# Kernel tuning notes

Hardware: AMD Instinct MI355X
Metric: run time of the kernel (lower is better)

The kernel has to match this reference:

```python
import jax, jax.numpy as jnp
import numpy as np

N = 16384
D_IN = 128
LAYERS = [128, 128, 128, 10]
LATENT = [64, 64]


def _linear_params(key, fan_in, fan_out):
    k1, k2 = jax.random.split(key)
    bound = 1.0 / np.sqrt(fan_in)
    w = jax.random.uniform(k1, (fan_in, fan_out), minval=-bound, maxval=bound, dtype=jnp.float32)
    b = jax.random.uniform(k2, (fan_out,), minval=-bound, maxval=bound, dtype=jnp.float32)
    return w, b


def setup_inputs() -> dict:
    key = jax.random.key(0)
    ks = jax.random.split(key, 8)
    feat_matrix = jax.random.normal(ks[0], (N, D_IN), dtype=jnp.float32)
    gl_w0, gl_b0 = _linear_params(ks[1], LAYERS[0], LATENT[0])
    gnn_w0, gnn_b0 = _linear_params(ks[2], LAYERS[0], LAYERS[1])
    gl_w1, gl_b1 = _linear_params(ks[3], LAYERS[1], LATENT[1])
    gnn_w1, gnn_b1 = _linear_params(ks[4], LAYERS[1], LAYERS[2])
    out_w, out_b = _linear_params(ks[5], LAYERS[2], LAYERS[3])
    return {
        "feat_matrix": feat_matrix,
        "gl_w0": gl_w0, "gl_b0": gl_b0,
        "gl_w1": gl_w1, "gl_b1": gl_b1,
        "gnn_w0": gnn_w0, "gnn_b0": gnn_b0,
        "gnn_w1": gnn_w1, "gnn_b1": gnn_b1,
        "out_w": out_w, "out_b": out_b,
        "temp": jnp.float32(0.1),
        "theta": jnp.float32(0.1),
        "adj_matrix": jnp.zeros((N, N), dtype=jnp.float32),
        "get_item_index": jax.random.randint(ks[6], (1024,), 0, N, dtype=jnp.int32),
        "set_index": jax.random.randint(ks[7], (1024,), 0, N, dtype=jnp.int32),
        "val_index": jax.random.randint(jax.random.fold_in(key, 9), (1024,), 0, N, dtype=jnp.int32),
        "mask_matrix": jnp.zeros((N,), dtype=bool),
    }


def _layer(x, gl_w, gl_b, gnn_w, gnn_b, temp, theta):
    # graph-learning projection
    g = jax.nn.relu(x @ gl_w + gl_b)                     # [N, L]
    # pairwise squared L2 distances (utils.l2_mat)
    sq = jnp.sum(g * g, axis=-1)                         # [N]
    dist = sq[:, None] + sq[None, :] - 2.0 * (g @ g.T)   # [N, N]
    t = 1.0 + temp
    th = 5.0 + theta
    adj = jax.nn.sigmoid(t * (-dist) + th)               # [N, N]
    # diag(rowsum).inverse() @ adj @ gnn(x) == row-normalized message passing
    msg = adj @ (x @ gnn_w + gnn_b)                      # [N, H]
    return msg / jnp.sum(adj, axis=-1, keepdims=True)


def reference(feat_matrix, gl_w0, gl_b0, gl_w1, gl_b1,
              gnn_w0, gnn_b0, gnn_w1, gnn_b1,
              out_w, out_b, temp, theta,
              adj_matrix, get_item_index, set_index, val_index, mask_matrix):
    x = feat_matrix
    x = jax.nn.relu(_layer(x, gl_w0, gl_b0, gnn_w0, gnn_b0, temp, theta))
    x = _layer(x, gl_w1, gl_b1, gnn_w1, gnn_b1, temp, theta)  # last gnn layer: no relu
    x = x @ out_w + out_b
    return jax.nn.softmax(x, axis=-1)
```

## Files before the change

### kernel.cpp

```cpp
#include <hip/hip_runtime.h>

#define NN 16384
#define DL 64
#define HD 128
#define BMW 32
#define BM 128
#define BN 64
#define JS 8
#define JCH (NN / JS)

typedef _Float16 v8h __attribute__((ext_vector_type(8)));
typedef float v16f __attribute__((ext_vector_type(16)));
typedef unsigned short ushort_t;
typedef unsigned int uint32;

__device__ __forceinline__ float bf2f(ushort_t v) {
  return __uint_as_float(((uint32)v) << 16);
}
__device__ __forceinline__ ushort_t f2bf(float f) {
  uint32 u = __float_as_uint(f);
  return (ushort_t)((u + 0x7FFFu + ((u >> 16) & 1u)) >> 16);
}
__device__ __forceinline__ uint32 pack2h(float a, float b) {
  union { _Float16 h; ushort_t s; } ua, ub;
  ua.h = (_Float16)a; ub.h = (_Float16)b;
  return (uint32)ua.s | ((uint32)ub.s << 16);
}
__device__ __forceinline__ void gld16(void* lds, const void* gp) {
  __builtin_amdgcn_global_load_lds(
      (const __attribute__((address_space(1))) uint32*)gp,
      (__attribute__((address_space(3))) uint32*)lds, 16, 0, 0);
}

__global__ void detect_k(const void* __restrict__ feat,
                         const void* __restrict__ temp,
                         const void* __restrict__ theta,
                         float* __restrict__ consts) {
  const int l = threadIdx.x;
  const ushort_t* u = (const ushort_t*)feat;
  float v0 = fabsf(bf2f(u[2 * l]));
  float v1 = fabsf(bf2f(u[2 * l + 1]));
  int ok = ((v0 > 1e-4f && v0 < 16.0f) ? 1 : 0) +
           ((v1 > 1e-4f && v1 < 16.0f) ? 1 : 0);
#pragma unroll
  for (int off = 1; off < 64; off <<= 1) ok += __shfl_xor(ok, off, 64);
  if (l == 0) {
    int isbf = (ok >= 100) ? 1 : 0;
    float tv, th;
    if (isbf) {
      tv = bf2f(((const ushort_t*)temp)[0]);
      th = bf2f(((const ushort_t*)theta)[0]);
    } else {
      tv = ((const float*)temp)[0];
      th = ((const float*)theta)[0];
    }
    consts[0] = (float)isbf;
    consts[1] = 1.0f + tv;
    consts[2] = 5.0f + th;
    consts[3] = 2.0f * (1.0f + tv) * 1.44269504088896341f;
  }
}

template <int L0>
__global__ __launch_bounds__(256) void prep_k(
    const void* __restrict__ xb, const float* __restrict__ msgp,
    const float* __restrict__ denp, const void* __restrict__ glw,
    const void* __restrict__ glb, const void* __restrict__ gnw,
    const void* __restrict__ gnb, const float* __restrict__ cst,
    _Float16* __restrict__ g, _Float16* __restrict__ hT,
    float* __restrict__ crow) {
  __shared__ float xr[4][128];
  const int w = threadIdx.x >> 6, l = threadIdx.x & 63;
  const int row = blockIdx.x * 4 + w;
  const int isbf = (cst[0] != 0.0f);
  float x0, x1;
  if (L0) {
    if (isbf) {
      const ushort_t* p = (const ushort_t*)xb;
      x0 = bf2f(p[row * 128 + 2 * l]);
      x1 = bf2f(p[row * 128 + 2 * l + 1]);
    } else {
      const float* p = (const float*)xb;
      x0 = p[row * 128 + 2 * l];
      x1 = p[row * 128 + 2 * l + 1];
    }
  } else {
    float m0 = 0.0f, m1 = 0.0f, d = 0.0f;
#pragma unroll
    for (int js = 0; js < JS; ++js) {
      const float* mp = msgp + (size_t)js * NN * HD + (size_t)row * HD;
      m0 += mp[2 * l];
      m1 += mp[2 * l + 1];
      d += denp[js * NN + row];
    }
    float rd = __builtin_amdgcn_rcpf(fmaxf(d, 1e-10f));
    x0 = fmaxf(m0 * rd, 0.0f);
    x1 = fmaxf(m1 * rd, 0.0f);
  }
  xr[w][2 * l] = x0;
  xr[w][2 * l + 1] = x1;
  __syncthreads();
  float ag = 0.0f, a0 = 0.0f, a1 = 0.0f;
  float bg, b0, b1;
  if (isbf) {
    const ushort_t* Wg = (const ushort_t*)glw;
    const ushort_t* Wn = (const ushort_t*)gnw;
#pragma unroll 8
    for (int k = 0; k < 128; ++k) {
      float xk = xr[w][k];
      ag = fmaf(xk, bf2f(Wg[k * 64 + l]), ag);
      a0 = fmaf(xk, bf2f(Wn[k * 128 + l]), a0);
      a1 = fmaf(xk, bf2f(Wn[k * 128 + 64 + l]), a1);
    }
    bg = bf2f(((const ushort_t*)glb)[l]);
    b0 = bf2f(((const ushort_t*)gnb)[l]);
    b1 = bf2f(((const ushort_t*)gnb)[64 + l]);
  } else {
    const float* Wg = (const float*)glw;
    const float* Wn = (const float*)gnw;
#pragma unroll 8
    for (int k = 0; k < 128; ++k) {
      float xk = xr[w][k];
      ag = fmaf(xk, Wg[k * 64 + l], ag);
      a0 = fmaf(xk, Wn[k * 128 + l], a0);
      a1 = fmaf(xk, Wn[k * 128 + 64 + l], a1);
    }
    bg = ((const float*)glb)[l];
    b0 = ((const float*)gnb)[l];
    b1 = ((const float*)gnb)[64 + l];
  }
  const float t = cst[1];
  const float th = cst[2];
  float gv = fmaxf(ag + bg, 0.0f);
  _Float16 gq = (_Float16)gv;
  g[(size_t)row * DL + l] = gq;
  float gf = (float)gq;
  float sq = gf * gf;
#pragma unroll
  for (int off = 1; off < 64; off <<= 1) sq += __shfl_xor(sq, off, 64);
  if (l == 0) crow[row] = (0.5f * th - t * sq) * 1.44269504088896341f;
  hT[(size_t)l * NN + row] = (_Float16)(a0 + b0);
  hT[(size_t)(l + 64) * NN + row] = (_Float16)(a1 + b1);
}

__global__ __launch_bounds__(256, 2) void attn_main(
    const _Float16* __restrict__ g, const _Float16* __restrict__ hT,
    const float* __restrict__ crow, const float* __restrict__ cst,
    float* __restrict__ msgp, float* __restrict__ denp) {
  __shared__ __align__(16) short SM[4096 + 8192];
  _Float16* Gs = (_Float16*)SM;
  _Float16* Hs = (_Float16*)(SM + 4096);

  const int tid = threadIdx.x;
  const int w = tid >> 6;
  const int l = tid & 63;
  const int ln = l & 31;
  const int hb = l >> 5;
  const int iw = blockIdx.x * BM + w * BMW;
  const int jb = blockIdx.y * JCH;
  const float s2 = cst[3];

  v8h Bi[4];
#pragma unroll
  for (int kf = 0; kf < 4; ++kf)
    Bi[kf] = *(const v8h*)(g + (size_t)(iw + ln) * DL + kf * 16 + hb * 8);

  const float ci = crow[iw + ln];

  v16f o[4];
#pragma unroll
  for (int mp = 0; mp < 4; ++mp)
#pragma unroll
    for (int r = 0; r < 16; ++r) o[mp][r] = 0.0f;

  float dp = 0.0f;

#pragma unroll 1
  for (int itr = 0; itr < JCH / BN; ++itr) {
    const int j0 = jb + itr * BN;
    __syncthreads();
#pragma unroll
    for (int oo = 0; oo < 2; ++oo) {
      int c = oo * 256 + tid;
      int jj = c >> 3, pc = c & 7;
      int kc = pc ^ (jj & 7);
      gld16((char*)Gs + (oo * 256 + w * 64) * 16,
            g + (size_t)(j0 + jj) * DL + kc * 8);
    }
#pragma unroll
    for (int oo = 0; oo < 4; ++oo) {
      int c = oo * 256 + tid;
      int hc = c >> 3, pc = c & 7;
      int jc = pc ^ (hc & 7);
      gld16((char*)Hs + (oo * 256 + w * 64) * 16,
            hT + (size_t)hc * NN + j0 + jc * 8);
    }
    __syncthreads();

#pragma unroll
    for (int jt = 0; jt < 2; ++jt) {
      float cj[16];
#pragma unroll
      for (int q2 = 0; q2 < 4; ++q2) {
        float4 f4 = *(const float4*)(crow + j0 + jt * 32 + q2 * 8 + 4 * hb);
        cj[q2 * 4 + 0] = f4.x;
        cj[q2 * 4 + 1] = f4.y;
        cj[q2 * 4 + 2] = f4.z;
        cj[q2 * 4 + 3] = f4.w;
      }
      v16f sv;
#pragma unroll
      for (int r = 0; r < 16; ++r) sv[r] = 0.0f;
#pragma unroll
      for (int kf = 0; kf < 4; ++kf) {
        int row = jt * 32 + ln;
        int kc = kf * 2 + hb;
        v8h a = *(const v8h*)(Gs + row * 64 + ((kc ^ (row & 7)) * 8));
        sv = __builtin_amdgcn_mfma_f32_32x32x16_f16(a, Bi[kf], sv, 0, 0, 0);
      }
      float pv[16];
      float dps = 0.0f;
#pragma unroll
      for (int r = 0; r < 16; ++r) {
        float arg = fmaf(s2, sv[r], ci) + cj[r];
        arg = fminf(fmaxf(arg, -60.0f), 60.0f);
        float e = __builtin_amdgcn_exp2f(-arg);
        float adj = 256.0f * __builtin_amdgcn_rcpf(1.0f + e);
        dps += adj;
        pv[r] = adj;
      }
      dp += dps;
#pragma unroll
      for (int kq = 0; kq < 2; ++kq) {
        int q = kq * 8;
        uint32 lo0 = pack2h(pv[q + 0], pv[q + 1]);
        uint32 lo1 = pack2h(pv[q + 2], pv[q + 3]);
        uint32 hi0 = pack2h(pv[q + 4], pv[q + 5]);
        uint32 hi1 = pack2h(pv[q + 6], pv[q + 7]);
        uint32 sl0 = (uint32)__shfl_xor((int)lo0, 32, 64);
        uint32 sl1 = (uint32)__shfl_xor((int)lo1, 32, 64);
        uint32 sh0 = (uint32)__shfl_xor((int)hi0, 32, 64);
        uint32 sh1 = (uint32)__shfl_xor((int)hi1, 32, 64);
        union { uint32 u[4]; v8h v; } b;
        b.u[0] = hb ? sh0 : lo0;
        b.u[1] = hb ? sh1 : lo1;
        b.u[2] = hb ? hi0 : sl0;
        b.u[3] = hb ? hi1 : sl1;
        int kc = (jt * 2 + kq) * 2 + hb;
#pragma unroll
        for (int mp = 0; mp < 4; ++mp) {
          int hc = mp * 32 + ln;
          v8h Ah = *(const v8h*)(Hs + hc * 64 + ((kc ^ (hc & 7)) * 8));
          o[mp] = __builtin_amdgcn_mfma_f32_32x32x16_f16(Ah, b.v, o[mp], 0, 0, 0);
        }
      }
    }
  }

  dp += __shfl_xor(dp, 32, 64);
  if (hb == 0) denp[blockIdx.y * NN + iw + ln] = dp;
  __syncthreads();
  float* Tw = ((float*)SM) + w * (32 * 33);
  float* mout = msgp + (size_t)blockIdx.y * NN * HD;
#pragma unroll
  for (int mp = 0; mp < 4; ++mp) {
#pragma unroll
    for (int r = 0; r < 16; ++r) {
      int hl = (r & 3) + 8 * (r >> 2) + 4 * hb;
      Tw[ln * 33 + hl] = o[mp][r];
    }
#pragma unroll
    for (int rr = 0; rr < 16; ++rr) {
      int il = rr * 2 + hb;
      mout[(size_t)(iw + il) * HD + mp * 32 + ln] = Tw[il * 33 + ln];
    }
  }
}

__global__ __launch_bounds__(256) void final_k(
    const float* __restrict__ msgp, const float* __restrict__ denp,
    const void* __restrict__ ow, const void* __restrict__ ob,
    const float* __restrict__ cst, void* __restrict__ out) {
  __shared__ float Ws[1280];
  const int isbf = (cst[0] != 0.0f);
  if (isbf) {
    for (int i = threadIdx.x; i < 1280; i += 256) Ws[i] = bf2f(((const ushort_t*)ow)[i]);
  } else {
    for (int i = threadIdx.x; i < 1280; i += 256) Ws[i] = ((const float*)ow)[i];
  }
  __syncthreads();
  const int l16 = threadIdx.x & 15, grp = threadIdx.x >> 4;
  const int row = blockIdx.x * 16 + grp;
  float d = 0.0f;
#pragma unroll
  for (int js = 0; js < JS; ++js) d += denp[js * NN + row];
  const float rd = __builtin_amdgcn_rcpf(fmaxf(d, 1e-10f));
  float acc[10];
#pragma unroll
  for (int c = 0; c < 10; ++c) acc[c] = 0.0f;
#pragma unroll
  for (int kk = 0; kk < 8; ++kk) {
    int k = kk * 16 + l16;
    float m = 0.0f;
#pragma unroll
    for (int js = 0; js < JS; ++js)
      m += msgp[(size_t)js * NN * HD + (size_t)row * HD + k];
    float xv = m * rd;
    xv = fminf(fmaxf(xv, -1e6f), 1e6f);
#pragma unroll
    for (int c = 0; c < 10; ++c) acc[c] = fmaf(xv, Ws[k * 10 + c], acc[c]);
  }
  float bias[10];
  if (isbf) {
#pragma unroll
    for (int c = 0; c < 10; ++c) bias[c] = bf2f(((const ushort_t*)ob)[c]);
  } else {
#pragma unroll
    for (int c = 0; c < 10; ++c) bias[c] = ((const float*)ob)[c];
  }
#pragma unroll
  for (int c = 0; c < 10; ++c) {
#pragma unroll
    for (int off = 1; off < 16; off <<= 1) acc[c] += __shfl_xor(acc[c], off, 64);
    acc[c] += bias[c];
  }
  float m = acc[0];
#pragma unroll
  for (int c = 1; c < 10; ++c) m = fmaxf(m, acc[c]);
  float s = 0.0f, e[10];
#pragma unroll
  for (int c = 0; c < 10; ++c) {
    e[c] = __builtin_amdgcn_exp2f((acc[c] - m) * 1.44269504088896341f);
    s += e[c];
  }
  float rs = __builtin_amdgcn_rcpf(s);
  float mine = e[0];
#pragma unroll
  for (int c = 1; c < 10; ++c) mine = (l16 == c) ? e[c] : mine;
  if (l16 < 10) {
    float v = mine * rs;
    if (isbf) ((ushort_t*)out)[(size_t)row * 10 + l16] = f2bf(v);
    else ((float*)out)[(size_t)row * 10 + l16] = v;
  }
}

extern "C" void kernel_launch(void* const* d_in, const int* in_sizes, int n_in,
                              void* d_out, int out_size, void* d_ws,
                              size_t ws_size, hipStream_t stream) {
  const void* feat = d_in[0];
  const void* glw0 = d_in[1];
  const void* glb0 = d_in[2];
  const void* glw1 = d_in[3];
  const void* glb1 = d_in[4];
  const void* gnw0 = d_in[5];
  const void* gnb0 = d_in[6];
  const void* gnw1 = d_in[7];
  const void* gnb1 = d_in[8];
  const void* ow = d_in[9];
  const void* obv = d_in[10];
  const void* temp = d_in[11];
  const void* thet = d_in[12];

  char* ws = (char*)d_ws;
  _Float16* g = (_Float16*)ws;
  _Float16* hT = (_Float16*)(ws + (size_t)(2u << 20));
  float* crow = (float*)(ws + (size_t)(6u << 20));
  float* cst = (float*)(ws + (size_t)(6u << 20) + (1u << 16));
  float* msgp = (float*)(ws + (size_t)(7u << 20));
  float* denp = (float*)(ws + (size_t)(71u << 20));

  dim3 b256(256);
  detect_k<<<dim3(1), dim3(64), 0, stream>>>(feat, temp, thet, cst);
  prep_k<1><<<dim3(NN / 4), b256, 0, stream>>>(feat, nullptr, nullptr, glw0,
                                               glb0, gnw0, gnb0, cst, g, hT,
                                               crow);
  attn_main<<<dim3(NN / BM, JS), b256, 0, stream>>>(g, hT, crow, cst, msgp,
                                                    denp);
  prep_k<0><<<dim3(NN / 4), b256, 0, stream>>>(nullptr, msgp, denp, glw1, glb1,
                                               gnw1, gnb1, cst, g, hT, crow);
  attn_main<<<dim3(NN / BM, JS), b256, 0, stream>>>(g, hT, crow, cst, msgp,
                                                    denp);
  final_k<<<dim3(NN / 16), b256, 0, stream>>>(msgp, denp, ow, obv, cst, d_out);
}
```

Measured before the change: 1.675 ms.

## Double-buffer LDS tiles in attention loop and cheapen sigmoid packing

Splits shared memory into two buffers so the async global-to-LDS loads for the next j-tile are issued before computing the current one. This hides load latency behind the MFMA and exp work and cuts one barrier per iteration. The change also packs to fp16 with a single round-toward-zero convert instruction and drops the clamp on the sigmoid argument. In exchange, LDS use per block doubles, which could limit occupancy. Skipping the clamp relies on exp2 overflow to infinity still giving a correct sigmoid.

```diff
diff --git a/kernel.cpp b/kernel.cpp
--- a/kernel.cpp
+++ b/kernel.cpp
@@ -8,8 +8,10 @@
 #define BN 64
 #define JS 8
 #define JCH (NN / JS)
+#define NITER (JCH / BN)
 
 typedef _Float16 v8h __attribute__((ext_vector_type(8)));
+typedef __fp16 v2fp16 __attribute__((ext_vector_type(2)));
 typedef float v16f __attribute__((ext_vector_type(16)));
 typedef unsigned short ushort_t;
 typedef unsigned int uint32;
@@ -22,9 +24,9 @@
   return (ushort_t)((u + 0x7FFFu + ((u >> 16) & 1u)) >> 16);
 }
 __device__ __forceinline__ uint32 pack2h(float a, float b) {
-  union { _Float16 h; ushort_t s; } ua, ub;
-  ua.h = (_Float16)a; ub.h = (_Float16)b;
-  return (uint32)ua.s | ((uint32)ub.s << 16);
+  union { v2fp16 h; uint32 u; } p;
+  p.h = __builtin_amdgcn_cvt_pkrtz(a, b);
+  return p.u;
 }
 __device__ __forceinline__ void gld16(void* lds, const void* gp) {
   __builtin_amdgcn_global_load_lds(
@@ -147,9 +149,7 @@
     const _Float16* __restrict__ g, const _Float16* __restrict__ hT,
     const float* __restrict__ crow, const float* __restrict__ cst,
     float* __restrict__ msgp, float* __restrict__ denp) {
-  __shared__ __align__(16) short SM[4096 + 8192];
-  _Float16* Gs = (_Float16*)SM;
-  _Float16* Hs = (_Float16*)(SM + 4096);
+  __shared__ __align__(16) short SM[2 * 12288];
 
   const int tid = threadIdx.x;
   const int w = tid >> 6;
@@ -175,27 +175,35 @@
 
   float dp = 0.0f;
 
-#pragma unroll 1
-  for (int itr = 0; itr < JCH / BN; ++itr) {
-    const int j0 = jb + itr * BN;
-    __syncthreads();
+  auto stage = [&](int p, int j0) {
+    char* Gb = (char*)(SM + p * 12288);
+    char* Hb = (char*)(SM + p * 12288 + 4096);
 #pragma unroll
     for (int oo = 0; oo < 2; ++oo) {
       int c = oo * 256 + tid;
       int jj = c >> 3, pc = c & 7;
       int kc = pc ^ (jj & 7);
-      gld16((char*)Gs + (oo * 256 + w * 64) * 16,
-            g + (size_t)(j0 + jj) * DL + kc * 8);
+      gld16(Gb + (oo * 256 + w * 64) * 16, g + (size_t)(j0 + jj) * DL + kc * 8);
     }
 #pragma unroll
     for (int oo = 0; oo < 4; ++oo) {
       int c = oo * 256 + tid;
       int hc = c >> 3, pc = c & 7;
       int jc = pc ^ (hc & 7);
-      gld16((char*)Hs + (oo * 256 + w * 64) * 16,
-            hT + (size_t)hc * NN + j0 + jc * 8);
-    }
+      gld16(Hb + (oo * 256 + w * 64) * 16, hT + (size_t)hc * NN + j0 + jc * 8);
+    }
+  };
+
+  stage(0, jb);
+
+#pragma unroll 1
+  for (int itr = 0; itr < NITER; ++itr) {
+    const int j0 = jb + itr * BN;
+    const int p = itr & 1;
     __syncthreads();
+    if (itr + 1 < NITER) stage(p ^ 1, j0 + BN);
+    _Float16* Gs = (_Float16*)(SM + p * 12288);
+    _Float16* Hs = (_Float16*)(SM + p * 12288 + 4096);
 
 #pragma unroll
     for (int jt = 0; jt < 2; ++jt) {
@@ -223,7 +231,6 @@
 #pragma unroll
       for (int r = 0; r < 16; ++r) {
         float arg = fmaf(s2, sv[r], ci) + cj[r];
-        arg = fminf(fmaxf(arg, -60.0f), 60.0f);
         float e = __builtin_amdgcn_exp2f(-arg);
         float adj = 256.0f * __builtin_amdgcn_rcpf(1.0f + e);
         dps += adj;
```

After: 1.582 ms. -5.6%, faster.
